# Performance work log

Hardware: AMD Instinct MI355X
Metric: run time of the kernel (lower is better)

The kernel has to match this reference:

```python
import jax, jax.numpy as jnp
import numpy as np

MIN_NORM = 1e-15
PROJ_EPS = 4e-3   # HGCN PoincareBall eps for float32
C = 1.0
N_NODES = 100000
DEG = 5
F_IN = 128


def _artanh(x):
    return jnp.arctanh(jnp.clip(x, -1.0 + 1e-7, 1.0 - 1e-7))


def _norm(x):
    # clamped L2 norm over last dim, keepdims
    return jnp.maximum(jnp.sqrt(jnp.sum(x * x, axis=-1, keepdims=True)), MIN_NORM)


def proj(x, c):
    norm = _norm(x)
    maxnorm = (1.0 - PROJ_EPS) / jnp.sqrt(c)
    return jnp.where(norm > maxnorm, x / norm * maxnorm, x)


def expmap0(u, c):
    sc = jnp.sqrt(c)
    un = _norm(u)
    return jnp.tanh(sc * un) * u / (sc * un)


def logmap0(p, c):
    sc = jnp.sqrt(c)
    pn = _norm(p)
    return p / pn / sc * _artanh(sc * pn)


def mobius_matvec(m, x, c):
    # HGCN convention: mx = x @ m^T
    sc = jnp.sqrt(c)
    x_norm = _norm(x)
    mx = x @ m.T
    mx_norm = _norm(mx)
    res = jnp.tanh(mx_norm / x_norm * _artanh(sc * x_norm)) * mx / (mx_norm * sc)
    zero = jnp.all(mx == 0, axis=-1, keepdims=True)
    return jnp.where(zero, jnp.zeros_like(res), res)


def setup_inputs() -> dict:
    key = jax.random.key(0)
    k1, k2, k3, k4 = jax.random.split(key, 4)
    x = jax.random.normal(k1, (N_NODES, F_IN), jnp.float32) * 0.1
    gain = 1.414
    W = jax.random.normal(k2, (F_IN, F_IN), jnp.float32) * gain * np.sqrt(2.0 / (F_IN + F_IN))
    a = jax.random.normal(k3, (1, 2 * F_IN), jnp.float32) * gain * np.sqrt(2.0 / (1 + 2 * F_IN))
    # edge list: every node has DEG out-edges so row-sum normalization is safe
    src = jnp.repeat(jnp.arange(N_NODES, dtype=jnp.int32), DEG)
    dst = jax.random.randint(k4, (N_NODES * DEG,), 0, N_NODES, jnp.int32)
    edge = jnp.stack([src, dst])  # [2, E]
    return {"x": x, "edge": edge, "W": W, "a": a}


def reference(x, edge, W, a):
    c = C
    N = x.shape[0]
    # h = logmap0(proj(mobius_matvec(x, W)))  -> [F, N] (module's transposed layout)
    h = logmap0(proj(mobius_matvec(x, W, c), c), c)
    src, dst = edge[0], edge[1]
    # per-edge gather: [2F, E]
    edge_h = jnp.concatenate([h[:, src], h[:, dst]], axis=0)
    edge_h = proj(expmap0(edge_h, c), c)
    # mobius_matvec(edge_h.T, a) -> a @ edge_h : [1, E] -> [E]
    ee = jnp.squeeze(mobius_matvec(edge_h.T, a, c))
    ee = logmap0(proj(ee, c), c)
    ee = jnp.exp(-jax.nn.gelu(ee, approximate=False))  # positive edge weights
    # sparse spmm row-sum and aggregation (scatter-add by source node)
    e_rowsum = jax.ops.segment_sum(ee, src, num_segments=N)                     # [N]
    h_prime = jax.ops.segment_sum(ee[:, None] * h.T[dst], src, num_segments=N)  # [N, F]
    h_prime = h_prime / e_rowsum[:, None]
    return proj(expmap0(jax.nn.elu(h_prime), c), c)
```

## Files before the change

### kernel.cpp

```cpp
#include <hip/hip_runtime.h>
#include <math.h>

#define F 128
#define DEG 5
#define TM 128
#define MAXNORM_D 0.996
#define MIN_NORM_D 1e-15

typedef float f32x4 __attribute__((ext_vector_type(4)));
typedef short s16x8 __attribute__((ext_vector_type(8)));
typedef _Float16 f16x4 __attribute__((ext_vector_type(4)));

__device__ inline double atanh_clip(double v) {
    v = fmin(fmax(v, -1.0 + 1e-7), 1.0 - 1e-7);
    return atanh(v);
}

__device__ inline void load_lds16(const void* g, void* l) {
    __builtin_amdgcn_global_load_lds((const __attribute__((address_space(1))) void*)g,
                                     (__attribute__((address_space(3))) void*)l, 16, 0, 0);
}

__device__ inline void split2(float v0, float v1, unsigned& hi, unsigned& lo) {
    unsigned b0 = __float_as_uint(v0), b1 = __float_as_uint(v1);
    unsigned h0 = (b0 + 0x8000u) >> 16;
    unsigned h1 = (b1 + 0x8000u) >> 16;
    float l0 = v0 - __uint_as_float(h0 << 16);
    float l1 = v1 - __uint_as_float(h1 << 16);
    hi = h0 | (h1 << 16);
    lo = (__float_as_uint(l0) >> 16) | (__float_as_uint(l1) & 0xFFFF0000u);
}

__global__ __launch_bounds__(256) void k_ph(const float* __restrict__ W,
                                            uint4* __restrict__ Wfh, uint4* __restrict__ Wfl,
                                            const int* __restrict__ edge, int* __restrict__ cnt, int E) {
    if (blockIdx.x < 8) {
        int tid = blockIdx.x * 256 + threadIdx.x;
        int c = tid >> 9;
        int tp = (tid >> 6) & 7;
        int lane = tid & 63;
        int f = tp * 16 + (lane & 15);
        int k = c * 32 + (lane >> 4) * 8;
        const float* wp = W + f * F + k;
        unsigned h[4], l[4];
#pragma unroll
        for (int p = 0; p < 4; p++) split2(wp[2 * p], wp[2 * p + 1], h[p], l[p]);
        Wfh[tid] = make_uint4(h[0], h[1], h[2], h[3]);
        Wfl[tid] = make_uint4(l[0], l[1], l[2], l[3]);
    } else {
        int stride = (gridDim.x - 8) * 256;
        for (int e = (blockIdx.x - 8) * 256 + threadIdx.x; e < E; e += stride)
            atomicAdd(&cnt[edge[E + e]], 1);
    }
}

__global__ __launch_bounds__(512, 4) void k_gemm(const float* __restrict__ x,
                                                 const uint4* __restrict__ Wfh, const uint4* __restrict__ Wfl,
                                                 const int* __restrict__ cnt, _Float16* __restrict__ yh,
                                                 float* __restrict__ ssum2, float* __restrict__ wsum2, int N) {
    __shared__ uint4 Wh_s[2048];
    __shared__ uint4 Wl_s[2048];
    __shared__ float red_ss[F];
    __shared__ float red_ws[F];
    __shared__ int cntL[TM];

    int t = threadIdx.x;
    int lane = t & 63;
    int w = t >> 6;
    int n0 = blockIdx.x * TM;

    if (t < F) { red_ss[t] = 0.f; red_ws[t] = 0.f; }
    if (t < TM) { int n = n0 + t; cntL[t] = (n < N) ? cnt[n] : 0; }

#pragma unroll
    for (int r = 0; r < 4; r++) {
        int off = (r * 512 + t) * 16;
        load_lds16((const char*)Wfh + off, (char*)Wh_s + off);
    }
#pragma unroll
    for (int r = 0; r < 4; r++) {
        int off = (r * 512 + t) * 16;
        load_lds16((const char*)Wfl + off, (char*)Wl_s + off);
    }

    int row = n0 + w * 16 + (lane & 15);
    if (row > N - 1) row = N - 1;
    const float* xr = x + (size_t)row * F + (lane >> 4) * 8;

    float4 av0[4], av1[4];
#pragma unroll
    for (int c = 0; c < 4; c++) {
        av0[c] = *(const float4*)(xr + c * 32);
        av1[c] = *(const float4*)(xr + c * 32 + 4);
    }

    f32x4 acc[8];
#pragma unroll
    for (int i = 0; i < 8; i++) acc[i] = (f32x4){0.f, 0.f, 0.f, 0.f};

    __syncthreads();

#pragma unroll
    for (int c = 0; c < 4; c++) {
        unsigned h[4], l[4];
        split2(av0[c].x, av0[c].y, h[0], l[0]);
        split2(av0[c].z, av0[c].w, h[1], l[1]);
        split2(av1[c].x, av1[c].y, h[2], l[2]);
        split2(av1[c].z, av1[c].w, h[3], l[3]);
        s16x8 a_hi = __builtin_bit_cast(s16x8, make_uint4(h[0], h[1], h[2], h[3]));
        s16x8 a_lo = __builtin_bit_cast(s16x8, make_uint4(l[0], l[1], l[2], l[3]));
#pragma unroll
        for (int tp = 0; tp < 8; tp++) {
            s16x8 bh = __builtin_bit_cast(s16x8, Wh_s[(c * 8 + tp) * 64 + lane]);
            s16x8 bl = __builtin_bit_cast(s16x8, Wl_s[(c * 8 + tp) * 64 + lane]);
            acc[tp] = __builtin_amdgcn_mfma_f32_16x16x32_bf16(a_hi, bh, acc[tp], 0, 0, 0);
            acc[tp] = __builtin_amdgcn_mfma_f32_16x16x32_bf16(a_lo, bh, acc[tp], 0, 0, 0);
            acc[tp] = __builtin_amdgcn_mfma_f32_16x16x32_bf16(a_hi, bl, acc[tp], 0, 0, 0);
        }
    }

    int fb = lane & 15;
    int rg = lane >> 4;
    int odd = fb & 1;

#pragma unroll
    for (int tp = 0; tp < 8; tp++) {
        int f = tp * 16 + fb;
        float sv = 0.f, wv = 0.f;
#pragma unroll
        for (int r = 0; r < 4; r++) {
            int lr = w * 16 + rg * 4 + r;
            int n = n0 + lr;
            float v = acc[tp][r];
            if (n < N) {
                sv += v * v;
                wv += (float)cntL[lr] * v * v;
            }
        }
        sv += __shfl_xor(sv, 16, 64); sv += __shfl_xor(sv, 32, 64);
        wv += __shfl_xor(wv, 16, 64); wv += __shfl_xor(wv, 32, 64);
        if (lane < 16) {
            atomicAdd(&red_ss[f], sv);
            atomicAdd(&red_ws[f], wv);
        }
    }

#pragma unroll
    for (int r = 0; r < 4; r++) {
        int n = n0 + w * 16 + rg * 4 + r;
        unsigned hb[8], ob[8], pk[8];
#pragma unroll
        for (int tp = 0; tp < 8; tp++) {
            _Float16 hv = (_Float16)acc[tp][r];
            hb[tp] = (unsigned)__builtin_bit_cast(unsigned short, hv);
        }
#pragma unroll
        for (int tp = 0; tp < 8; tp++) ob[tp] = (unsigned)__shfl_xor((int)hb[tp], 1, 64);
#pragma unroll
        for (int tp = 0; tp < 8; tp++)
            pk[tp] = odd ? (ob[tp] | (hb[tp] << 16)) : (hb[tp] | (ob[tp] << 16));
        if (n < N) {
            unsigned* bp = (unsigned*)(yh + (size_t)n * F + (fb & ~1));
#pragma unroll
            for (int i = 0; i < 4; i++) {
                int tp = 2 * i + odd;
                unsigned v = odd ? pk[2 * i + 1] : pk[2 * i];
                bp[tp * 8] = v;
            }
        }
    }

    __syncthreads();
    if (t < F) {
        int bank = (blockIdx.x & 7) * F;
        atomicAdd(&ssum2[bank + t], red_ss[t]);
        atomicAdd(&wsum2[bank + t], red_ws[t]);
    }
}

__global__ __launch_bounds__(256) void k_scalars(const float* __restrict__ W, const float* __restrict__ a,
                                                 const float* __restrict__ ssum2, const float* __restrict__ wsum2,
                                                 float* __restrict__ s_arr, float* __restrict__ asrc,
                                                 float* __restrict__ adst, double* __restrict__ an_out) {
    int t = threadIdx.x;
    double av = (double)a[t];
    av *= av;
#pragma unroll
    for (int off = 32; off; off >>= 1) av += __shfl_down(av, off, 64);
    __shared__ double wred[4];
    if ((t & 63) == 0) wred[t >> 6] = av;
    __syncthreads();
    double an = fmax(sqrt(wred[0] + wred[1] + wred[2] + wred[3]), MIN_NORM_D);
    if (t == 0) an_out[0] = an;

    if (t < F) {
        float ss2f = 0.f, ws2f = 0.f;
#pragma unroll
        for (int b = 0; b < 8; b++) { ss2f += ssum2[b * F + t]; ws2f += wsum2[b * F + t]; }

        double wn2 = 0.0;
        for (int k = 0; k < F; k++) { double w = (double)W[t * F + k]; wn2 += w * w; }
        double wn = fmax(sqrt(wn2), MIN_NORM_D);
        double mxnf = fmax(sqrt((double)ss2f), MIN_NORM_D);
        double tt = tanh(mxnf / wn * atanh_clip(wn));
        double rn = fmax(tt, MIN_NORM_D);
        double pf = (rn > MAXNORM_D) ? MAXNORM_D / rn : 1.0;
        double pn = rn * pf;
        double s = (tt / mxnf) * pf * atanh_clip(pn) / pn;
        s_arr[t] = (float)s;

        double un_s = fmax(s * sqrt((double)DEG * (double)ss2f), MIN_NORM_D);
        double th_s = tanh(un_s);
        double rn2 = fmax(th_s, MIN_NORM_D);
        double pf2 = (rn2 > MAXNORM_D) ? MAXNORM_D / rn2 : 1.0;
        double q_s = s * (th_s / un_s) * pf2;
        asrc[t] = (float)((double)a[t] * q_s);

        double un_d = fmax(s * sqrt((double)ws2f), MIN_NORM_D);
        double th_d = tanh(un_d);
        double rn3 = fmax(th_d, MIN_NORM_D);
        double pf3 = (rn3 > MAXNORM_D) ? MAXNORM_D / rn3 : 1.0;
        double q_d = s * (th_d / un_d) * pf3;
        adst[t] = (float)((double)a[F + t] * q_d);
    }
}

__global__ __launch_bounds__(256) void k_pq(const _Float16* __restrict__ yh, const float* __restrict__ asrc,
                                            const float* __restrict__ adst, float* __restrict__ P,
                                            float* __restrict__ Q, int N) {
    __shared__ float as4[F], ad4[F];
    int t = threadIdx.x;
    if (t < F) { as4[t] = asrc[t]; ad4[t] = adst[t]; }
    __syncthreads();
    int lane = t & 31;
    float4 av = *(const float4*)&as4[lane * 4];
    float4 bv = *(const float4*)&ad4[lane * 4];
    for (int nb = blockIdx.x * 8; nb < N; nb += gridDim.x * 8) {
        int n = nb + (t >> 5);
        if (n < N) {
            f16x4 hv = *(const f16x4*)&yh[(size_t)n * F + lane * 4];
            float4 yv = make_float4((float)hv[0], (float)hv[1], (float)hv[2], (float)hv[3]);
            float p = yv.x * av.x + yv.y * av.y + yv.z * av.z + yv.w * av.w;
            float q = yv.x * bv.x + yv.y * bv.y + yv.z * bv.z + yv.w * bv.w;
#pragma unroll
            for (int off = 16; off; off >>= 1) {
                p += __shfl_down(p, off, 32);
                q += __shfl_down(q, off, 32);
            }
            if (lane == 0) { P[n] = p; Q[n] = q; }
        }
    }
}

__global__ __launch_bounds__(256) void k_edge(const int* __restrict__ edge, const float* __restrict__ P,
                                              const float* __restrict__ Q,
                                              double* __restrict__ mxn2, int E) {
    int t = threadIdx.x;
    double local = 0.0;
    for (int e0 = blockIdx.x * 256; e0 < E; e0 += gridDim.x * 256) {
        int e = e0 + t;
        if (e < E) {
            float v = P[e / DEG] + Q[edge[E + e]];
            local += (double)v * (double)v;
        }
    }
#pragma unroll
    for (int off = 32; off; off >>= 1) local += __shfl_down(local, off, 64);
    __shared__ double wsum[4];
    if ((t & 63) == 0) wsum[t >> 6] = local;
    __syncthreads();
    if (t == 0) atomicAdd(mxn2, wsum[0] + wsum[1] + wsum[2] + wsum[3]);
}

__global__ __launch_bounds__(256) void k_wagg(const int* __restrict__ edge, const _Float16* __restrict__ yh,
                                              const float* __restrict__ P, const float* __restrict__ Q,
                                              const double* __restrict__ an_p, const double* __restrict__ mxn2_p,
                                              const float* __restrict__ s_arr,
                                              float* __restrict__ out, int N, int E) {
    __shared__ float gS;
    int t = threadIdx.x;
    if (t == 0) {
        double an = an_p[0];
        double mxn = fmax(sqrt(mxn2_p[0]), MIN_NORM_D);
        double t2 = tanh(mxn / an * atanh_clip(an));
        double f2 = t2 / mxn;
        double rnp = fmax(t2, MIN_NORM_D);
        double pfp = (rnp > MAXNORM_D) ? MAXNORM_D / rnp : 1.0;
        double pnp = rnp * pfp;
        gS = (float)(f2 * pfp * atanh_clip(pnp) / pnp);
    }
    __syncthreads();
    float g = gS;

    int lane = t & 63;
    int sub = lane & 7;
    int slot = t >> 3;
    int gbase = lane & ~7;

    int n = blockIdx.x * 32 + slot;
    bool active = (n < N);
    int nc = active ? n : N - 1;

    float w = 0.f; int d = 0;
    if (sub < DEG) {
        int e = nc * DEG + sub;
        int dn = edge[E + e];
        float v = P[nc] + Q[dn];
        float xg = g * v;
        float gl = 0.5f * xg * (1.f + erff(xg * 0.70710678f));
        w = expf(-gl);
        d = dn << 7;
    }
    float wj[DEG]; int dj[DEG];
#pragma unroll
    for (int j = 0; j < DEG; j++) {
        wj[j] = __shfl(w, gbase + j, 64);
        dj[j] = __shfl(d, gbase + j, 64);
    }
    float rowsum = wj[0] + wj[1] + wj[2] + wj[3] + wj[4];
    float inv = 1.f / rowsum;

    float4 acc[4];
#pragma unroll
    for (int p = 0; p < 4; p++) acc[p] = make_float4(0.f, 0.f, 0.f, 0.f);
#pragma unroll
    for (int j = 0; j < DEG; j++) {
        const _Float16* yp = yh + dj[j] + sub * 4;
        float wv = wj[j];
#pragma unroll
        for (int p = 0; p < 4; p++) {
            f16x4 hv = *(const f16x4*)(yp + p * 32);
            acc[p].x = fmaf(wv, (float)hv[0], acc[p].x);
            acc[p].y = fmaf(wv, (float)hv[1], acc[p].y);
            acc[p].z = fmaf(wv, (float)hv[2], acc[p].z);
            acc[p].w = fmaf(wv, (float)hv[3], acc[p].w);
        }
    }

    float4 s4[4];
#pragma unroll
    for (int p = 0; p < 4; p++) s4[p] = *(const float4*)&s_arr[p * 32 + sub * 4];

    float4 el[4];
    float ss = 0.f;
#pragma unroll
    for (int p = 0; p < 4; p++) {
        float h;
        h = s4[p].x * acc[p].x * inv; el[p].x = (h > 0.f) ? h : expm1f(h);
        h = s4[p].y * acc[p].y * inv; el[p].y = (h > 0.f) ? h : expm1f(h);
        h = s4[p].z * acc[p].z * inv; el[p].z = (h > 0.f) ? h : expm1f(h);
        h = s4[p].w * acc[p].w * inv; el[p].w = (h > 0.f) ? h : expm1f(h);
        ss += el[p].x * el[p].x + el[p].y * el[p].y + el[p].z * el[p].z + el[p].w * el[p].w;
    }
    ss += __shfl_xor(ss, 1, 64);
    ss += __shfl_xor(ss, 2, 64);
    ss += __shfl_xor(ss, 4, 64);

    float un = fmaxf(sqrtf(ss), 1e-15f);
    float th = tanhf(un);
    float sc = th / un;
    float rn = fmaxf(th, 1e-15f);
    if (rn > 0.996f) sc *= 0.996f / rn;
    if (active) {
        float* op = out + (size_t)n * F + sub * 4;
#pragma unroll
        for (int p = 0; p < 4; p++) {
            float4 o = make_float4(el[p].x * sc, el[p].y * sc, el[p].z * sc, el[p].w * sc);
            *(float4*)(op + p * 32) = o;
        }
    }
}

extern "C" void kernel_launch(void* const* d_in, const int* in_sizes, int n_in,
                              void* d_out, int out_size, void* d_ws, size_t ws_size,
                              hipStream_t stream) {
    const float* x = (const float*)d_in[0];
    const int* edge = (const int*)d_in[1];
    const float* W = (const float*)d_in[2];
    const float* a = (const float*)d_in[3];
    float* out = (float*)d_out;
    int N = in_sizes[0] / F;
    int E = in_sizes[1] / 2;

    char* ws = (char*)d_ws;
    size_t off = 0;
    _Float16* yh = (_Float16*)(ws + off); off += (size_t)N * F * 2;
    uint4* Wfh = (uint4*)(ws + off);     off += 2048 * 16;
    uint4* Wfl = (uint4*)(ws + off);     off += 2048 * 16;
    float* P = (float*)(ws + off);       off += (size_t)N * 4;
    float* Q = (float*)(ws + off);       off += (size_t)N * 4;
    char* zbase = ws + off;
    int* cnt = (int*)(ws + off);         off += (size_t)N * 4;
    float* ssum2 = (float*)(ws + off);   off += 8 * F * 4;
    float* wsum2 = (float*)(ws + off);   off += 8 * F * 4;
    double* mxn2 = (double*)(ws + off);  off += 8;
    size_t zlen = (size_t)((ws + off) - zbase);
    double* an_p = (double*)(ws + off);  off += 8;
    float* s_arr = (float*)(ws + off);   off += 512;
    float* asrc = (float*)(ws + off);    off += 512;
    float* adst = (float*)(ws + off);    off += 512;

    hipMemsetAsync(zbase, 0, zlen, stream);
    k_ph<<<8 + 1024, 256, 0, stream>>>(W, Wfh, Wfl, edge, cnt, E);
    k_gemm<<<(N + TM - 1) / TM, 512, 0, stream>>>(x, Wfh, Wfl, cnt, yh, ssum2, wsum2, N);
    k_scalars<<<1, 256, 0, stream>>>(W, a, ssum2, wsum2, s_arr, asrc, adst, an_p);
    k_pq<<<2048, 256, 0, stream>>>(yh, asrc, adst, P, Q, N);
    k_edge<<<1024, 256, 0, stream>>>(edge, P, Q, mxn2, E);
    k_wagg<<<(N + 31) / 32, 256, 0, stream>>>(edge, yh, P, Q, an_p, mxn2, s_arr, out, N, E);
}
```

Measured before the change: 212.9 us.

## Halve GEMM weight LDS footprint by staging W in two halves

The GEMM kernel now keeps only half of the split bf16 weight matrix (hi/lo) in shared memory at a time: it loads the first K-half, runs two MFMA chunks, syncs, reloads the second half and runs the remaining chunks. LDS use per block drops from about 64KB to about 32KB, and launch bounds ask for 8 blocks per CU instead of 4, aiming for higher occupancy to hide latency. The cost is two extra barriers and a serialized second weight load that is not overlapped with compute. The tighter launch bound may also force register spills.

```diff
diff --git a/kernel.cpp b/kernel.cpp
--- a/kernel.cpp
+++ b/kernel.cpp
@@ -29,6 +29,26 @@
     float l1 = v1 - __uint_as_float(h1 << 16);
     hi = h0 | (h1 << 16);
     lo = (__float_as_uint(l0) >> 16) | (__float_as_uint(l1) & 0xFFFF0000u);
+}
+
+__device__ inline void mfma_chunk(const float4& a0, const float4& a1,
+                                  const uint4* Wh_s, const uint4* Wl_s,
+                                  int cc, int lane, f32x4* acc) {
+    unsigned h[4], l[4];
+    split2(a0.x, a0.y, h[0], l[0]);
+    split2(a0.z, a0.w, h[1], l[1]);
+    split2(a1.x, a1.y, h[2], l[2]);
+    split2(a1.z, a1.w, h[3], l[3]);
+    s16x8 a_hi = __builtin_bit_cast(s16x8, make_uint4(h[0], h[1], h[2], h[3]));
+    s16x8 a_lo = __builtin_bit_cast(s16x8, make_uint4(l[0], l[1], l[2], l[3]));
+#pragma unroll
+    for (int tp = 0; tp < 8; tp++) {
+        s16x8 bh = __builtin_bit_cast(s16x8, Wh_s[(cc * 8 + tp) * 64 + lane]);
+        s16x8 bl = __builtin_bit_cast(s16x8, Wl_s[(cc * 8 + tp) * 64 + lane]);
+        acc[tp] = __builtin_amdgcn_mfma_f32_16x16x32_bf16(a_hi, bh, acc[tp], 0, 0, 0);
+        acc[tp] = __builtin_amdgcn_mfma_f32_16x16x32_bf16(a_lo, bh, acc[tp], 0, 0, 0);
+        acc[tp] = __builtin_amdgcn_mfma_f32_16x16x32_bf16(a_hi, bl, acc[tp], 0, 0, 0);
+    }
 }
 
 __global__ __launch_bounds__(256) void k_ph(const float* __restrict__ W,
@@ -54,12 +74,12 @@
     }
 }
 
-__global__ __launch_bounds__(512, 4) void k_gemm(const float* __restrict__ x,
+__global__ __launch_bounds__(512, 8) void k_gemm(const float* __restrict__ x,
                                                  const uint4* __restrict__ Wfh, const uint4* __restrict__ Wfl,
                                                  const int* __restrict__ cnt, _Float16* __restrict__ yh,
                                                  float* __restrict__ ssum2, float* __restrict__ wsum2, int N) {
-    __shared__ uint4 Wh_s[2048];
-    __shared__ uint4 Wl_s[2048];
+    __shared__ uint4 Wh_s[1024];
+    __shared__ uint4 Wl_s[1024];
     __shared__ float red_ss[F];
     __shared__ float red_ws[F];
     __shared__ int cntL[TM];
@@ -73,12 +93,12 @@
     if (t < TM) { int n = n0 + t; cntL[t] = (n < N) ? cnt[n] : 0; }
 
 #pragma unroll
-    for (int r = 0; r < 4; r++) {
+    for (int r = 0; r < 2; r++) {
         int off = (r * 512 + t) * 16;
         load_lds16((const char*)Wfh + off, (char*)Wh_s + off);
     }
 #pragma unroll
-    for (int r = 0; r < 4; r++) {
+    for (int r = 0; r < 2; r++) {
         int off = (r * 512 + t) * 16;
         load_lds16((const char*)Wfl + off, (char*)Wl_s + off);
     }
@@ -100,24 +120,25 @@
 
     __syncthreads();
 
-#pragma unroll
-    for (int c = 0; c < 4; c++) {
-        unsigned h[4], l[4];
-        split2(av0[c].x, av0[c].y, h[0], l[0]);
-        split2(av0[c].z, av0[c].w, h[1], l[1]);
-        split2(av1[c].x, av1[c].y, h[2], l[2]);
-        split2(av1[c].z, av1[c].w, h[3], l[3]);
-        s16x8 a_hi = __builtin_bit_cast(s16x8, make_uint4(h[0], h[1], h[2], h[3]));
-        s16x8 a_lo = __builtin_bit_cast(s16x8, make_uint4(l[0], l[1], l[2], l[3]));
-#pragma unroll
-        for (int tp = 0; tp < 8; tp++) {
-            s16x8 bh = __builtin_bit_cast(s16x8, Wh_s[(c * 8 + tp) * 64 + lane]);
-            s16x8 bl = __builtin_bit_cast(s16x8, Wl_s[(c * 8 + tp) * 64 + lane]);
-            acc[tp] = __builtin_amdgcn_mfma_f32_16x16x32_bf16(a_hi, bh, acc[tp], 0, 0, 0);
-            acc[tp] = __builtin_amdgcn_mfma_f32_16x16x32_bf16(a_lo, bh, acc[tp], 0, 0, 0);
-            acc[tp] = __builtin_amdgcn_mfma_f32_16x16x32_bf16(a_hi, bl, acc[tp], 0, 0, 0);
-        }
-    }
+    mfma_chunk(av0[0], av1[0], Wh_s, Wl_s, 0, lane, acc);
+    mfma_chunk(av0[1], av1[1], Wh_s, Wl_s, 1, lane, acc);
+
+    __syncthreads();
+
+#pragma unroll
+    for (int r = 0; r < 2; r++) {
+        int off = (r * 512 + t) * 16;
+        load_lds16((const char*)Wfh + 16384 + off, (char*)Wh_s + off);
+    }
+#pragma unroll
+    for (int r = 0; r < 2; r++) {
+        int off = (r * 512 + t) * 16;
+        load_lds16((const char*)Wfl + 16384 + off, (char*)Wl_s + off);
+    }
+    __syncthreads();
+
+    mfma_chunk(av0[2], av1[2], Wh_s, Wl_s, 0, lane, acc);
+    mfma_chunk(av0[3], av1[3], Wh_s, Wl_s, 1, lane, acc);
 
     int fb = lane & 15;
     int rg = lane >> 4;
```

Measured after the change: 223.2 us. 4.8% more time.

## Process two row tiles per block and prefetch second tile during first epilogue

Applied to the files above, without the earlier changes.

Doubles rows per block in the projection GEMM kernel, so each block handles two 128-row subtiles while reusing the W split loaded into LDS once. The x loads for the second subtile are issued before the first subtile's epilogue, so global-load latency overlaps with the stores and reductions. This halves the number of blocks, which cuts repeated W staging and global atomics, but it raises register pressure and may reduce parallelism and occupancy. Whether the cntL buffer was resized for the larger TM is not shown.

```diff
diff --git a/kernel.cpp b/kernel.cpp
--- a/kernel.cpp
+++ b/kernel.cpp
@@ -3,7 +3,7 @@
 
 #define F 128
 #define DEG 5
-#define TM 128
+#define TM 256
 #define MAXNORM_D 0.996
 #define MIN_NORM_D 1e-15
 
@@ -29,6 +29,82 @@
     float l1 = v1 - __uint_as_float(h1 << 16);
     hi = h0 | (h1 << 16);
     lo = (__float_as_uint(l0) >> 16) | (__float_as_uint(l1) & 0xFFFF0000u);
+}
+
+__device__ inline void mfma_tile(const float4* av0, const float4* av1,
+                                 const uint4* Wh_s, const uint4* Wl_s,
+                                 int lane, f32x4* acc) {
+#pragma unroll
+    for (int c = 0; c < 4; c++) {
+        unsigned h[4], l[4];
+        split2(av0[c].x, av0[c].y, h[0], l[0]);
+        split2(av0[c].z, av0[c].w, h[1], l[1]);
+        split2(av1[c].x, av1[c].y, h[2], l[2]);
+        split2(av1[c].z, av1[c].w, h[3], l[3]);
+        s16x8 a_hi = __builtin_bit_cast(s16x8, make_uint4(h[0], h[1], h[2], h[3]));
+        s16x8 a_lo = __builtin_bit_cast(s16x8, make_uint4(l[0], l[1], l[2], l[3]));
+#pragma unroll
+        for (int tp = 0; tp < 8; tp++) {
+            s16x8 bh = __builtin_bit_cast(s16x8, Wh_s[(c * 8 + tp) * 64 + lane]);
+            s16x8 bl = __builtin_bit_cast(s16x8, Wl_s[(c * 8 + tp) * 64 + lane]);
+            acc[tp] = __builtin_amdgcn_mfma_f32_16x16x32_bf16(a_hi, bh, acc[tp], 0, 0, 0);
+            acc[tp] = __builtin_amdgcn_mfma_f32_16x16x32_bf16(a_lo, bh, acc[tp], 0, 0, 0);
+            acc[tp] = __builtin_amdgcn_mfma_f32_16x16x32_bf16(a_hi, bl, acc[tp], 0, 0, 0);
+        }
+    }
+}
+
+__device__ inline void epilogue(const f32x4* acc, int nbase, const int* cntSub,
+                                _Float16* __restrict__ yh, float* red_ss, float* red_ws,
+                                int lane, int w, int N) {
+    int fb = lane & 15;
+    int rg = lane >> 4;
+    int odd = fb & 1;
+#pragma unroll
+    for (int tp = 0; tp < 8; tp++) {
+        int f = tp * 16 + fb;
+        float sv = 0.f, wv = 0.f;
+#pragma unroll
+        for (int r = 0; r < 4; r++) {
+            int lr = w * 16 + rg * 4 + r;
+            int n = nbase + lr;
+            float v = acc[tp][r];
+            if (n < N) {
+                sv += v * v;
+                wv += (float)cntSub[lr] * v * v;
+            }
+        }
+        sv += __shfl_xor(sv, 16, 64); sv += __shfl_xor(sv, 32, 64);
+        wv += __shfl_xor(wv, 16, 64); wv += __shfl_xor(wv, 32, 64);
+        if (lane < 16) {
+            atomicAdd(&red_ss[f], sv);
+            atomicAdd(&red_ws[f], wv);
+        }
+    }
+#pragma unroll
+    for (int r = 0; r < 4; r++) {
+        int n = nbase + w * 16 + rg * 4 + r;
+        unsigned hb[8], ob[8], pk[8];
+#pragma unroll
+        for (int tp = 0; tp < 8; tp++) {
+            _Float16 hv = (_Float16)acc[tp][r];
+            hb[tp] = (unsigned)__builtin_bit_cast(unsigned short, hv);
+        }
+#pragma unroll
+        for (int tp = 0; tp < 8; tp++) ob[tp] = (unsigned)__shfl_xor((int)hb[tp], 1, 64);
+#pragma unroll
+        for (int tp = 0; tp < 8; tp++)
+            pk[tp] = odd ? (ob[tp] | (hb[tp] << 16)) : (hb[tp] | (ob[tp] << 16));
+        if (n < N) {
+            unsigned* bp = (unsigned*)(yh + (size_t)n * F + (fb & ~1));
+#pragma unroll
+            for (int i = 0; i < 4; i++) {
+                int tp = 2 * i + odd;
+                unsigned v = odd ? pk[2 * i + 1] : pk[2 * i];
+                bp[tp * 8] = v;
+            }
+        }
+    }
 }
 
 __global__ __launch_bounds__(256) void k_ph(const float* __restrict__ W,
@@ -83,92 +159,44 @@
         load_lds16((const char*)Wfl + off, (char*)Wl_s + off);
     }
 
-    int row = n0 + w * 16 + (lane & 15);
-    if (row > N - 1) row = N - 1;
-    const float* xr = x + (size_t)row * F + (lane >> 4) * 8;
-
-    float4 av0[4], av1[4];
-#pragma unroll
-    for (int c = 0; c < 4; c++) {
-        av0[c] = *(const float4*)(xr + c * 32);
-        av1[c] = *(const float4*)(xr + c * 32 + 4);
-    }
-
-    f32x4 acc[8];
-#pragma unroll
-    for (int i = 0; i < 8; i++) acc[i] = (f32x4){0.f, 0.f, 0.f, 0.f};
-
-    __syncthreads();
-
-#pragma unroll
-    for (int c = 0; c < 4; c++) {
-        unsigned h[4], l[4];
-        split2(av0[c].x, av0[c].y, h[0], l[0]);
-        split2(av0[c].z, av0[c].w, h[1], l[1]);
-        split2(av1[c].x, av1[c].y, h[2], l[2]);
-        split2(av1[c].z, av1[c].w, h[3], l[3]);
-        s16x8 a_hi = __builtin_bit_cast(s16x8, make_uint4(h[0], h[1], h[2], h[3]));
-        s16x8 a_lo = __builtin_bit_cast(s16x8, make_uint4(l[0], l[1], l[2], l[3]));
-#pragma unroll
-        for (int tp = 0; tp < 8; tp++) {
-            s16x8 bh = __builtin_bit_cast(s16x8, Wh_s[(c * 8 + tp) * 64 + lane]);
-            s16x8 bl = __builtin_bit_cast(s16x8, Wl_s[(c * 8 + tp) * 64 + lane]);
-            acc[tp] = __builtin_amdgcn_mfma_f32_16x16x32_bf16(a_hi, bh, acc[tp], 0, 0, 0);
-            acc[tp] = __builtin_amdgcn_mfma_f32_16x16x32_bf16(a_lo, bh, acc[tp], 0, 0, 0);
-            acc[tp] = __builtin_amdgcn_mfma_f32_16x16x32_bf16(a_hi, bl, acc[tp], 0, 0, 0);
-        }
-    }
-
     int fb = lane & 15;
     int rg = lane >> 4;
-    int odd = fb & 1;
-
-#pragma unroll
-    for (int tp = 0; tp < 8; tp++) {
-        int f = tp * 16 + fb;
-        float sv = 0.f, wv = 0.f;
-#pragma unroll
-        for (int r = 0; r < 4; r++) {
-            int lr = w * 16 + rg * 4 + r;
-            int n = n0 + lr;
-            float v = acc[tp][r];
-            if (n < N) {
-                sv += v * v;
-                wv += (float)cntL[lr] * v * v;
-            }
-        }
-        sv += __shfl_xor(sv, 16, 64); sv += __shfl_xor(sv, 32, 64);
-        wv += __shfl_xor(wv, 16, 64); wv += __shfl_xor(wv, 32, 64);
-        if (lane < 16) {
-            atomicAdd(&red_ss[f], sv);
-            atomicAdd(&red_ws[f], wv);
-        }
-    }
-
-#pragma unroll
-    for (int r = 0; r < 4; r++) {
-        int n = n0 + w * 16 + rg * 4 + r;
-        unsigned hb[8], ob[8], pk[8];
-#pragma unroll
-        for (int tp = 0; tp < 8; tp++) {
-            _Float16 hv = (_Float16)acc[tp][r];
-            hb[tp] = (unsigned)__builtin_bit_cast(unsigned short, hv);
-        }
-#pragma unroll
-        for (int tp = 0; tp < 8; tp++) ob[tp] = (unsigned)__shfl_xor((int)hb[tp], 1, 64);
-#pragma unroll
-        for (int tp = 0; tp < 8; tp++)
-            pk[tp] = odd ? (ob[tp] | (hb[tp] << 16)) : (hb[tp] | (ob[tp] << 16));
-        if (n < N) {
-            unsigned* bp = (unsigned*)(yh + (size_t)n * F + (fb & ~1));
-#pragma unroll
-            for (int i = 0; i < 4; i++) {
-                int tp = 2 * i + odd;
-                unsigned v = odd ? pk[2 * i + 1] : pk[2 * i];
-                bp[tp * 8] = v;
-            }
-        }
-    }
+
+    int row1 = n0 + w * 16 + fb;
+    if (row1 > N - 1) row1 = N - 1;
+    const float* xr1 = x + (size_t)row1 * F + rg * 8;
+    float4 av0[4], av1[4];
+#pragma unroll
+    for (int c = 0; c < 4; c++) {
+        av0[c] = *(const float4*)(xr1 + c * 32);
+        av1[c] = *(const float4*)(xr1 + c * 32 + 4);
+    }
+
+    f32x4 acc[8];
+#pragma unroll
+    for (int i = 0; i < 8; i++) acc[i] = (f32x4){0.f, 0.f, 0.f, 0.f};
+
+    __syncthreads();
+
+    mfma_tile(av0, av1, Wh_s, Wl_s, lane, acc);
+
+    int row2 = n0 + 128 + w * 16 + fb;
+    if (row2 > N - 1) row2 = N - 1;
+    const float* xr2 = x + (size_t)row2 * F + rg * 8;
+    float4 bv0[4], bv1[4];
+#pragma unroll
+    for (int c = 0; c < 4; c++) {
+        bv0[c] = *(const float4*)(xr2 + c * 32);
+        bv1[c] = *(const float4*)(xr2 + c * 32 + 4);
+    }
+
+    epilogue(acc, n0, cntL, yh, red_ss, red_ws, lane, w, N);
+
+#pragma unroll
+    for (int i = 0; i < 8; i++) acc[i] = (f32x4){0.f, 0.f, 0.f, 0.f};
+    mfma_tile(bv0, bv1, Wh_s, Wl_s, lane, acc);
+
+    epilogue(acc, n0 + 128, cntL + 128, yh, red_ss, red_ws, lane, w, N);
 
     __syncthreads();
     if (t < F) {
```

Measured after the change: 210.3 us. Within noise of the previous version (-1.2%).
